# Performance work log

Hardware: AMD Instinct MI355X
Metric: run time of the kernel (lower is better)

Reference implementation:

```python
import jax, jax.numpy as jnp
import numpy as np

N = 50000      # nodes
E = 400000     # edges (before self loops)
IN = 128       # in_channels
H = 4          # num_heads (layers 1-2)
C = 32         # hidden_dim per head
HID = H * C    # 128 total hidden
CLS = 40       # num_classes (out_heads = 1)
EPS = 1e-5     # BatchNorm eps
SLOPE = 0.2    # LeakyReLU negative slope (PyG GATConv default)


def setup_inputs() -> dict:
    key = jax.random.key(0)
    ks = jax.random.split(key, 24)
    rn = lambda k, shp, s: jax.random.normal(k, shp, jnp.float32) * s
    x = jax.random.normal(ks[0], (N, IN), jnp.float32)
    src = jax.random.randint(ks[1], (E,), 0, N)
    dst = jax.random.randint(ks[2], (E,), 0, N)
    src = jnp.where(src == dst, (src + 1) % N, src)  # no pre-existing self loops
    edge_index = jnp.stack([src, dst]).astype(jnp.int32)
    inp = dict(x=x, edge_index=edge_index)
    # conv1: in IN -> H heads x C
    inp['W1'] = rn(ks[3], (IN, H * C), 1.0 / np.sqrt(IN))
    inp['as1'] = rn(ks[4], (H, C), 0.1)
    inp['ad1'] = rn(ks[5], (H, C), 0.1)
    inp['b1'] = rn(ks[6], (H * C,), 0.02)
    # conv2: HID -> H x C
    inp['W2'] = rn(ks[7], (HID, H * C), 1.0 / np.sqrt(HID))
    inp['as2'] = rn(ks[8], (H, C), 0.1)
    inp['ad2'] = rn(ks[9], (H, C), 0.1)
    inp['b2'] = rn(ks[10], (H * C,), 0.02)
    # conv3: HID -> 1 head x CLS, concat=False
    inp['W3'] = rn(ks[11], (HID, CLS), 1.0 / np.sqrt(HID))
    inp['as3'] = rn(ks[12], (1, CLS), 0.1)
    inp['ad3'] = rn(ks[13], (1, CLS), 0.1)
    inp['b3'] = rn(ks[14], (CLS,), 0.02)
    # residual projection
    inp['Wres'] = rn(ks[15], (IN, HID), 1.0 / np.sqrt(IN))
    # BatchNorm (eval mode: running stats)
    inp['g1'] = 1.0 + rn(ks[16], (HID,), 0.1)
    inp['be1'] = rn(ks[17], (HID,), 0.1)
    inp['m1'] = rn(ks[18], (HID,), 0.1)
    inp['v1'] = 1.0 + jax.random.uniform(ks[19], (HID,), jnp.float32) * 0.5
    inp['g2'] = 1.0 + rn(ks[20], (HID,), 0.1)
    inp['be2'] = rn(ks[21], (HID,), 0.1)
    inp['m2'] = rn(ks[22], (HID,), 0.1)
    inp['v2'] = 1.0 + jax.random.uniform(ks[23], (HID,), jnp.float32) * 0.5
    return inp


def _gat_conv(h, src, dst, W, a_src, a_dst, bias, heads, out_ch, concat):
    """PyG-style GATConv (eval: attention dropout off), self loops already in src/dst."""
    n = h.shape[0]
    xw = (h @ W).reshape(n, heads, out_ch)                    # [N,H,C]
    e_src = jnp.sum(xw * a_src, axis=-1)                      # [N,H]
    e_dst = jnp.sum(xw * a_dst, axis=-1)                      # [N,H]
    e = jax.nn.leaky_relu(e_src[src] + e_dst[dst], SLOPE)     # [E',H]
    # segment softmax over incoming edges of each dst node
    mseg = jax.ops.segment_max(e, dst, num_segments=n)        # [N,H]
    ex = jnp.exp(e - mseg[dst])
    den = jax.ops.segment_sum(ex, dst, num_segments=n)
    alpha = ex / den[dst]                                     # [E',H]
    out = jax.ops.segment_sum(alpha[:, :, None] * xw[src], dst, num_segments=n)  # [N,H,C]
    out = out.reshape(n, heads * out_ch) if concat else out.mean(axis=1)
    return out + bias


def _bn(h, g, b, m, v):
    return (h - m) * jax.lax.rsqrt(v + EPS) * g + b


def reference(x, edge_index, W1, as1, ad1, b1, W2, as2, ad2, b2,
              W3, as3, ad3, b3, Wres, g1, be1, m1, v1, g2, be2, m2, v2):
    n = x.shape[0]
    loop = jnp.arange(n, dtype=edge_index.dtype)
    src = jnp.concatenate([edge_index[0], loop])  # add self loops (PyG default)
    dst = jnp.concatenate([edge_index[1], loop])
    x0 = x
    h = _gat_conv(x0, src, dst, W1, as1, ad1, b1, H, C, True)
    h = jax.nn.elu(_bn(h, g1, be1, m1, v1) + x0 @ Wres)
    h_res = h
    h = _gat_conv(h, src, dst, W2, as2, ad2, b2, H, C, True)
    h = jax.nn.elu(_bn(h, g2, be2, m2, v2) + h_res)
    logits = _gat_conv(h, src, dst, W3, as3, ad3, b3, 1, CLS, False)
    return logits
```

## Files before the change

### kernel.cpp

```cpp
#include <hip/hip_runtime.h>
#include <hip/hip_bf16.h>

#define THREADS 256

typedef __attribute__((ext_vector_type(8))) short bfrag;
typedef __attribute__((ext_vector_type(4))) float f32x4;

__device__ inline unsigned short f2b(float v) {
    __hip_bfloat16 b = __float2bfloat16(v);
    return *reinterpret_cast<unsigned short*>(&b);
}
__device__ inline float b2f(unsigned short u) {
    return __uint_as_float(((unsigned)u) << 16);
}
__device__ inline float rdv(const void* p, int off, bool isbf) {
    return isbf ? b2f(((const unsigned short*)p)[off]) : ((const float*)p)[off];
}

__global__ void detect_kernel(const unsigned short* __restrict__ x, int n, int* flag) {
    __shared__ int cnt;
    if (threadIdx.x == 0) cnt = 0;
    __syncthreads();
    int local = 0;
    for (int i = threadIdx.x; i < n; i += THREADS) {
        unsigned ex = (x[i] >> 7) & 0xFF;
        if (ex == 0xFF || ex >= 134 || (ex > 0 && ex <= 100)) local++;
    }
    atomicAdd(&cnt, local);
    __syncthreads();
    if (threadIdx.x == 0) *flag = (cnt * 8 > n) ? 0 : 1;
}

struct InPtrs { const void* p[23]; };

__global__ void prep_kernel(InPtrs in, const int* __restrict__ flag,
                            unsigned short* __restrict__ Wl1, unsigned short* __restrict__ Wl2,
                            unsigned short* __restrict__ WlR, unsigned short* __restrict__ Wl3,
                            float* __restrict__ bnsc1, float* __restrict__ bnsh1,
                            float* __restrict__ bnsc2, float* __restrict__ bnsh2,
                            float* __restrict__ AS1f, float* __restrict__ AD1f,
                            float* __restrict__ AS2f, float* __restrict__ AD2f,
                            float* __restrict__ AS3f, float* __restrict__ AD3f,
                            float* __restrict__ B3f, unsigned short* __restrict__ xb,
                            int N, const int* __restrict__ ei, int* __restrict__ deg,
                            int E, int CB) {
    bool isbf = (*flag != 0);
    int b = blockIdx.x;
    if (b < 27) {
        const void* Wv; unsigned short* o; int cols, tt;
        if (b < 8)       { Wv = in.p[2];  o = Wl1; cols = 128; tt = b; }
        else if (b < 16) { Wv = in.p[6];  o = Wl2; cols = 128; tt = b - 8; }
        else if (b < 24) { Wv = in.p[14]; o = WlR; cols = 128; tt = b - 16; }
        else             { Wv = in.p[10]; o = Wl3; cols = 40;  tt = b - 24; }
        int id = tt * 256 + threadIdx.x;
        int t = id >> 8, ks = (id >> 6) & 3, l = id & 63;
        int q = l >> 4, n = l & 15;
        int c = t * 16 + n;
#pragma unroll
        for (int j = 0; j < 8; ++j) {
            int k = ks * 32 + q * 8 + j;
            float v = (c < cols) ? rdv(Wv, k * cols + c, isbf) : 0.f;
            o[id * 8 + j] = f2b(v);
        }
    } else if (b == 27) {
        int c = threadIdx.x;
        if (c < 128) {
            float s = rdv(in.p[15], c, isbf) * rsqrtf(rdv(in.p[18], c, isbf) + 1e-5f);
            bnsc1[c] = s;
            bnsh1[c] = rdv(in.p[16], c, isbf) - rdv(in.p[17], c, isbf) * s +
                       rdv(in.p[5], c, isbf) * s;
            AS1f[c] = rdv(in.p[3], c, isbf);
            AD1f[c] = rdv(in.p[4], c, isbf);
            AS2f[c] = rdv(in.p[7], c, isbf);
            AD2f[c] = rdv(in.p[8], c, isbf);
        } else {
            int d = c - 128;
            float s = rdv(in.p[19], d, isbf) * rsqrtf(rdv(in.p[22], d, isbf) + 1e-5f);
            bnsc2[d] = s;
            bnsh2[d] = rdv(in.p[20], d, isbf) - rdv(in.p[21], d, isbf) * s +
                       rdv(in.p[9], d, isbf) * s;
            if (d < 40) {
                AS3f[d] = rdv(in.p[11], d, isbf);
                AD3f[d] = rdv(in.p[12], d, isbf);
                B3f[d] = rdv(in.p[13], d, isbf);
            }
        }
    } else if (b < 28 + CB) {
        int i = (b - 28) * 256 + threadIdx.x;
        if (i < E + N) {
            int d = (i < E) ? ei[E + i] : (i - E);
            atomicAdd(&deg[d], 1);
        }
    } else {
        if (isbf) return;
        const float* xf = (const float*)in.p[0];
        int total = N * 128;
        int stride = (gridDim.x - 28 - CB) * 256;
        for (int i = (b - 28 - CB) * 256 + threadIdx.x; i < total; i += stride)
            xb[i] = f2b(xf[i]);
    }
}

__global__ void bsum_kernel(const int* __restrict__ deg, int* __restrict__ bsum, int N) {
    int idx = blockIdx.x * 256 + threadIdx.x;
    int lane = threadIdx.x & 63, wv = threadIdx.x >> 6;
    int v = (idx < N) ? deg[idx] : 0;
#pragma unroll
    for (int o = 1; o < 64; o <<= 1) v += __shfl_xor(v, o, 64);
    __shared__ int ws[4];
    if (lane == 0) ws[wv] = v;
    __syncthreads();
    if (threadIdx.x == 0) bsum[blockIdx.x] = ws[0] + ws[1] + ws[2] + ws[3];
}

__global__ __launch_bounds__(1024) void bscan_kernel(const int* __restrict__ bsum,
                                                     int* __restrict__ boff, int nb) {
    __shared__ int ws[16];
    int tid = threadIdx.x, lane = tid & 63, wv = tid >> 6;
    int v = (tid < nb) ? bsum[tid] : 0;
    int sc = v;
#pragma unroll
    for (int o = 1; o < 64; o <<= 1) {
        int t = __shfl_up(sc, o, 64);
        if (lane >= o) sc += t;
    }
    if (lane == 63) ws[wv] = sc;
    __syncthreads();
    int add = 0;
#pragma unroll
    for (int k = 0; k < 16; ++k) add += (k < wv) ? ws[k] : 0;
    if (tid < nb) boff[tid] = add + sc - v;
}

__global__ void scanw_kernel(const int* __restrict__ deg, const int* __restrict__ boff,
                             int* __restrict__ row_ptr, int* __restrict__ pos, int N) {
    int idx = blockIdx.x * 256 + threadIdx.x;
    int lane = threadIdx.x & 63, wv = threadIdx.x >> 6;
    int v = (idx < N) ? deg[idx] : 0;
    int sc = v;
#pragma unroll
    for (int o = 1; o < 64; o <<= 1) {
        int t = __shfl_up(sc, o, 64);
        if (lane >= o) sc += t;
    }
    __shared__ int ws[4];
    if (lane == 63) ws[wv] = sc;
    __syncthreads();
    int add = boff[blockIdx.x];
#pragma unroll
    for (int k = 0; k < 4; ++k) add += (k < wv) ? ws[k] : 0;
    int excl = add + sc - v;
    if (idx < N) {
        pos[idx] = excl;
        row_ptr[idx + 1] = excl + v;
    }
    if (idx == 0) row_ptr[0] = 0;
}

__global__ void scatter_kernel(const int* __restrict__ ei, int* __restrict__ pos,
                               int* __restrict__ csr, int E, int N) {
    int e = blockIdx.x * THREADS + threadIdx.x;
    if (e >= E + N) return;
    int s, d;
    if (e < E) { s = ei[e]; d = ei[E + e]; }
    else { s = e - E; d = s; }
    int p = atomicAdd(&pos[d], 1);
    csr[p] = s;
}

template <int COLT, int HEADS, bool ES>
__global__ __launch_bounds__(256) void gemm_mfma(
    const unsigned short* __restrict__ A, const unsigned short* __restrict__ Wg,
    const float* __restrict__ as_f, const float* __restrict__ ad_f,
    unsigned short* __restrict__ out, int ldc, int cols,
    float* __restrict__ es, float* __restrict__ ed, int N) {
    __shared__ __align__(16) unsigned short Wls[COLT * 2048];
    int tid = threadIdx.x;
    {
        const float4* src = (const float4*)Wg;
        float4* dst = (float4*)Wls;
#pragma unroll
        for (int i = 0; i < COLT; ++i) dst[tid + i * 256] = src[tid + i * 256];
    }
    __syncthreads();
    int w = tid >> 6, lane = tid & 63;
    int n = lane & 15, q = lane >> 4;
    int row0 = blockIdx.x * 64 + w * 16;
    int ar = row0 + n; ar = ar < N ? ar : N - 1;
    f32x4 acc[COLT];
#pragma unroll
    for (int t = 0; t < COLT; ++t) acc[t] = (f32x4){0.f, 0.f, 0.f, 0.f};
    const unsigned short* arow = A + (size_t)ar * 128;
#pragma unroll
    for (int ks = 0; ks < 4; ++ks) {
        bfrag a = *reinterpret_cast<const bfrag*>(arow + ks * 32 + q * 8);
#pragma unroll
        for (int t = 0; t < COLT; ++t) {
            bfrag b = *reinterpret_cast<const bfrag*>(&Wls[((t * 4 + ks) * 64 + lane) * 8]);
            acc[t] = __builtin_amdgcn_mfma_f32_16x16x32_bf16(a, b, acc[t], 0, 0, 0);
        }
    }
    if (ES) {
        float asv[COLT], adv[COLT];
#pragma unroll
        for (int t = 0; t < COLT; ++t) {
            int c = t * 16 + n;
            asv[t] = (c < cols) ? as_f[c] : 0.f;
            adv[t] = (c < cols) ? ad_f[c] : 0.f;
        }
#pragma unroll
        for (int r = 0; r < 4; ++r) {
            float pe[HEADS], pd[HEADS];
#pragma unroll
            for (int h = 0; h < HEADS; ++h) { pe[h] = 0.f; pd[h] = 0.f; }
#pragma unroll
            for (int t = 0; t < COLT; ++t) {
                int h = (HEADS == 4) ? (t >> 1) : 0;
                pe[h] = fmaf(acc[t][r], asv[t], pe[h]);
                pd[h] = fmaf(acc[t][r], adv[t], pd[h]);
            }
#pragma unroll
            for (int h = 0; h < HEADS; ++h) {
#pragma unroll
                for (int o = 1; o < 16; o <<= 1) {
                    pe[h] += __shfl_xor(pe[h], o, 64);
                    pd[h] += __shfl_xor(pd[h], o, 64);
                }
            }
            int row = row0 + q * 4 + r;
            if (n == 0 && row < N) {
#pragma unroll
                for (int h = 0; h < HEADS; ++h) {
                    es[(size_t)row * HEADS + h] = pe[h];
                    ed[(size_t)row * HEADS + h] = pd[h];
                }
            }
        }
    }
#pragma unroll
    for (int t = 0; t < COLT; ++t) {
        int col = t * 16 + n;
        if (col < cols) {
#pragma unroll
            for (int r = 0; r < 4; ++r) {
                int row = row0 + q * 4 + r;
                if (row < N) out[(size_t)row * ldc + col] = f2b(acc[t][r]);
            }
        }
    }
}

__global__ __launch_bounds__(256) void gemm_dual(
    const unsigned short* __restrict__ Araw, const unsigned short* __restrict__ Acvt,
    const int* __restrict__ flag,
    const unsigned short* __restrict__ Wg1, const unsigned short* __restrict__ WgR,
    const float* __restrict__ as_f, const float* __restrict__ ad_f,
    unsigned short* __restrict__ xwb, unsigned short* __restrict__ resb,
    float* __restrict__ es, float* __restrict__ ed, int N) {
    __shared__ __align__(16) unsigned short Wls[16 * 2048];
    int tid = threadIdx.x;
    {
        const float4* s1 = (const float4*)Wg1;
        const float4* s2 = (const float4*)WgR;
        float4* dst = (float4*)Wls;
#pragma unroll
        for (int i = 0; i < 8; ++i) dst[tid + i * 256] = s1[tid + i * 256];
#pragma unroll
        for (int i = 0; i < 8; ++i) dst[2048 + tid + i * 256] = s2[tid + i * 256];
    }
    const unsigned short* A = (*flag) ? Araw : Acvt;
    __syncthreads();
    int w = tid >> 6, lane = tid & 63;
    int n = lane & 15, q = lane >> 4;
    int row0 = blockIdx.x * 64 + w * 16;
    int ar = row0 + n; ar = ar < N ? ar : N - 1;
    f32x4 acc[16];
#pragma unroll
    for (int t = 0; t < 16; ++t) acc[t] = (f32x4){0.f, 0.f, 0.f, 0.f};
    const unsigned short* arow = A + (size_t)ar * 128;
#pragma unroll
    for (int ks = 0; ks < 4; ++ks) {
        bfrag a = *reinterpret_cast<const bfrag*>(arow + ks * 32 + q * 8);
#pragma unroll
        for (int t = 0; t < 8; ++t) {
            bfrag b = *reinterpret_cast<const bfrag*>(&Wls[((t * 4 + ks) * 64 + lane) * 8]);
            acc[t] = __builtin_amdgcn_mfma_f32_16x16x32_bf16(a, b, acc[t], 0, 0, 0);
        }
#pragma unroll
        for (int t = 0; t < 8; ++t) {
            bfrag b = *reinterpret_cast<const bfrag*>(&Wls[16384 + ((t * 4 + ks) * 64 + lane) * 8]);
            acc[8 + t] = __builtin_amdgcn_mfma_f32_16x16x32_bf16(a, b, acc[8 + t], 0, 0, 0);
        }
    }
    float asv[8], adv[8];
#pragma unroll
    for (int t = 0; t < 8; ++t) {
        int c = t * 16 + n;
        asv[t] = as_f[c];
        adv[t] = ad_f[c];
    }
#pragma unroll
    for (int r = 0; r < 4; ++r) {
        float pe[4] = {0.f, 0.f, 0.f, 0.f}, pd[4] = {0.f, 0.f, 0.f, 0.f};
#pragma unroll
        for (int t = 0; t < 8; ++t) {
            int h = t >> 1;
            pe[h] = fmaf(acc[t][r], asv[t], pe[h]);
            pd[h] = fmaf(acc[t][r], adv[t], pd[h]);
        }
#pragma unroll
        for (int h = 0; h < 4; ++h) {
#pragma unroll
            for (int o = 1; o < 16; o <<= 1) {
                pe[h] += __shfl_xor(pe[h], o, 64);
                pd[h] += __shfl_xor(pd[h], o, 64);
            }
        }
        int row = row0 + q * 4 + r;
        if (n == 0 && row < N) {
#pragma unroll
            for (int h = 0; h < 4; ++h) {
                es[(size_t)row * 4 + h] = pe[h];
                ed[(size_t)row * 4 + h] = pd[h];
            }
        }
    }
#pragma unroll
    for (int t = 0; t < 8; ++t) {
        int col = t * 16 + n;
#pragma unroll
        for (int r = 0; r < 4; ++r) {
            int row = row0 + q * 4 + r;
            if (row < N) {
                xwb[(size_t)row * 128 + col] = f2b(acc[t][r]);
                resb[(size_t)row * 128 + col] = f2b(acc[8 + t][r]);
            }
        }
    }
}

__global__ __launch_bounds__(256) void agg128_fused(
    const unsigned short* __restrict__ xwb, const float* __restrict__ es,
    const float* __restrict__ ed, const int* __restrict__ row_ptr,
    const int* __restrict__ csr, const float* __restrict__ bnsc,
    const float* __restrict__ bnsh, const unsigned short* __restrict__ resb,
    unsigned short* __restrict__ outb, int N) {
    int w = threadIdx.x >> 6, lane = threadIdx.x & 63;
    int node = blockIdx.x * 4 + w;
    if (node >= N) return;
    int h = lane >> 4;
    int c0 = lane * 2;
    float edl = ed[node * 4 + h];
    int start = __builtin_amdgcn_readfirstlane(row_ptr[node]);
    int end = __builtin_amdgcn_readfirstlane(row_ptr[node + 1]);
    float den = 0.f, a0 = 0.f, a1 = 0.f;
    for (int jb = start; jb < end; jb += 16) {
        int su[16];
#pragma unroll
        for (int u = 0; u < 16; ++u) {
            int idx = jb + u;
            idx = idx < end - 1 ? idx : end - 1;
            su[u] = csr[idx];
        }
        unsigned uu[16];
        float ev[16];
#pragma unroll
        for (int u = 0; u < 16; ++u) {
            uu[u] = *(const unsigned*)(xwb + (size_t)su[u] * 128 + c0);
            ev[u] = es[su[u] * 4 + h];
        }
#pragma unroll
        for (int u = 0; u < 16; ++u) {
            float e = ev[u] + edl;
            e = e > 0.f ? e : 0.2f * e;
            float wg = __expf(e);
            wg = (jb + u < end) ? wg : 0.f;
            den += wg;
            a0 = fmaf(wg, __uint_as_float(uu[u] << 16), a0);
            a1 = fmaf(wg, __uint_as_float(uu[u] & 0xffff0000u), a1);
        }
    }
    float inv = 1.f / den;
    float2 sc = *(const float2*)(bnsc + c0);
    float2 sh = *(const float2*)(bnsh + c0);
    unsigned ur = *(const unsigned*)(resb + (size_t)node * 128 + c0);
    float v0 = fmaf(a0 * inv, sc.x, sh.x) + __uint_as_float(ur << 16);
    float v1 = fmaf(a1 * inv, sc.y, sh.y) + __uint_as_float(ur & 0xffff0000u);
    v0 = v0 > 0.f ? v0 : expm1f(v0);
    v1 = v1 > 0.f ? v1 : expm1f(v1);
    unsigned pk = (unsigned)f2b(v0) | ((unsigned)f2b(v1) << 16);
    *(unsigned*)(outb + (size_t)node * 128 + c0) = pk;
}

__global__ __launch_bounds__(256) void agg40_kernel(
    const unsigned short* __restrict__ xw3b, const float* __restrict__ es3,
    const float* __restrict__ ed3, const int* __restrict__ row_ptr,
    const int* __restrict__ csr, const float* __restrict__ b3,
    void* __restrict__ out, const int* __restrict__ flag, int N) {
    int w = threadIdx.x >> 6, lane = threadIdx.x & 63;
    int node = blockIdx.x * 4 + w;
    if (node >= N) return;
    int i16 = lane & 15;
    int g = lane >= 40 ? 2 : (lane >= 20 ? 1 : 0);
    int cp = lane - g * 20;
    int c0 = cp * 2; c0 = c0 > 38 ? 38 : c0;
    float edl = ed3[node];
    int start = row_ptr[node], end = row_ptr[node + 1];
    float den = 0.f, a0 = 0.f, a1 = 0.f;
    for (int jb = start; jb < end; jb += 16) {
        int cnt = end - jb; cnt = cnt < 16 ? cnt : 16;
        int sv = csr[jb + (i16 < cnt ? i16 : 0)];
        unsigned uu[6];
#pragma unroll
        for (int t = 0; t < 6; ++t) {
            int slot = 3 * t + g; slot = slot < 15 ? slot : 15;
            int s = __shfl(sv, slot, 64);
            uu[t] = *(const unsigned*)(xw3b + (size_t)s * 40 + c0);
        }
        float wgl = 0.f;
        if (i16 < cnt) {
            float e = es3[sv] + edl;
            e = e > 0.f ? e : 0.2f * e;
            wgl = __expf(e);
        }
        float d = wgl;
        d += __shfl_xor(d, 1, 64);
        d += __shfl_xor(d, 2, 64);
        d += __shfl_xor(d, 4, 64);
        d += __shfl_xor(d, 8, 64);
        den += d;
#pragma unroll
        for (int t = 0; t < 6; ++t) {
            int slot = 3 * t + g;
            int sl = slot < 15 ? slot : 15;
            float wg = __shfl(wgl, sl, 64);
            if (slot >= cnt) wg = 0.f;
            a0 = fmaf(wg, __uint_as_float(uu[t] << 16), a0);
            a1 = fmaf(wg, __uint_as_float(uu[t] & 0xffff0000u), a1);
        }
    }
    float t0 = __shfl(a0, (lane + 20) & 63, 64);
    float t1 = __shfl(a0, (lane + 40) & 63, 64);
    float u0 = __shfl(a1, (lane + 20) & 63, 64);
    float u1 = __shfl(a1, (lane + 40) & 63, 64);
    a0 += t0 + t1;
    a1 += u0 + u1;
    if (lane < 20) {
        float inv = 1.f / den;
        float v0 = a0 * inv + b3[c0];
        float v1 = a1 * inv + b3[c0 + 1];
        size_t eoff = (size_t)node * 40 + c0;
        if (*flag) {
            unsigned pk = (unsigned)f2b(v0) | ((unsigned)f2b(v1) << 16);
            *(unsigned*)((unsigned short*)out + eoff) = pk;
        } else {
            *(float2*)((float*)out + eoff) = make_float2(v0, v1);
        }
    }
}

extern "C" void kernel_launch(void* const* d_in, const int* in_sizes, int n_in,
                              void* d_out, int out_size, void* d_ws, size_t ws_size,
                              hipStream_t stream) {
    (void)n_in; (void)out_size; (void)ws_size;
    const int N = in_sizes[0] / 128;
    const int E = in_sizes[1] / 2;
    const int EPN = E + N;
    const int NB = (N + 255) / 256;
    const int CB = (EPN + 255) / 256;
    char* base = (char*)d_ws;
    size_t off = 0;
    auto alloc = [&](size_t bytes) -> char* {
        char* p = base + off;
        off = (off + bytes + 255) & ~(size_t)255;
        return p;
    };
    int* flag = (int*)alloc(4);
    int* deg = (int*)alloc((size_t)N * 4);
    int* row_ptr = (int*)alloc((size_t)(N + 1) * 4);
    int* pos = (int*)alloc((size_t)N * 4);
    int* bsum = (int*)alloc((size_t)NB * 4);
    int* boff = (int*)alloc((size_t)NB * 4);
    int* csr = (int*)alloc((size_t)EPN * 4);
    float* bnsc1 = (float*)alloc(512); float* bnsh1 = (float*)alloc(512);
    float* bnsc2 = (float*)alloc(512); float* bnsh2 = (float*)alloc(512);
    float* AS1f = (float*)alloc(512); float* AD1f = (float*)alloc(512);
    float* AS2f = (float*)alloc(512); float* AD2f = (float*)alloc(512);
    float* AS3f = (float*)alloc(256); float* AD3f = (float*)alloc(256);
    float* B3f = (float*)alloc(256);
    unsigned short* Wl1 = (unsigned short*)alloc(32768);
    unsigned short* Wl2 = (unsigned short*)alloc(32768);
    unsigned short* WlR = (unsigned short*)alloc(32768);
    unsigned short* Wl3 = (unsigned short*)alloc(12288);
    unsigned short* xb = (unsigned short*)alloc((size_t)N * 128 * 2);
    unsigned short* xwb = (unsigned short*)alloc((size_t)N * 128 * 2);
    unsigned short* h1b = (unsigned short*)alloc((size_t)N * 128 * 2);
    unsigned short* resb = (unsigned short*)alloc((size_t)N * 128 * 2);
    float* es = (float*)alloc((size_t)N * 4 * 4);
    float* ed = (float*)alloc((size_t)N * 4 * 4);

    const int* ei = (const int*)d_in[1];

    hipMemsetAsync(deg, 0, (size_t)N * 4, stream);
    detect_kernel<<<1, THREADS, 0, stream>>>((const unsigned short*)d_in[0], 4096, flag);

    InPtrs ip;
    for (int t = 0; t < 23; t++) ip.p[t] = d_in[t];
    prep_kernel<<<28 + CB + 1024, THREADS, 0, stream>>>(ip, flag, Wl1, Wl2, WlR, Wl3,
                                                        bnsc1, bnsh1, bnsc2, bnsh2,
                                                        AS1f, AD1f, AS2f, AD2f,
                                                        AS3f, AD3f, B3f, xb, N, ei, deg, E, CB);

    bsum_kernel<<<NB, 256, 0, stream>>>(deg, bsum, N);
    bscan_kernel<<<1, 1024, 0, stream>>>(bsum, boff, NB);
    scanw_kernel<<<NB, 256, 0, stream>>>(deg, boff, row_ptr, pos, N);
    scatter_kernel<<<(EPN + THREADS - 1) / THREADS, THREADS, 0, stream>>>(ei, pos, csr, E, N);

    int gemmGrid = (N + 63) / 64;
    int aggGrid = (N + 3) / 4;

    gemm_dual<<<gemmGrid, 256, 0, stream>>>((const unsigned short*)d_in[0], xb, flag,
                                            Wl1, WlR, AS1f, AD1f, xwb, resb, es, ed, N);
    agg128_fused<<<aggGrid, 256, 0, stream>>>(xwb, es, ed, row_ptr, csr,
                                              bnsc1, bnsh1, resb, h1b, N);
    gemm_mfma<8, 4, true><<<gemmGrid, 256, 0, stream>>>(
        h1b, Wl2, AS2f, AD2f, xwb, 128, 128, es, ed, N);
    unsigned short* h2b = resb;
    agg128_fused<<<aggGrid, 256, 0, stream>>>(xwb, es, ed, row_ptr, csr,
                                              bnsc2, bnsh2, h1b, h2b, N);
    gemm_mfma<3, 1, true><<<gemmGrid, 256, 0, stream>>>(
        h2b, Wl3, AS3f, AD3f, xwb, 40, 40, es, ed, N);
    agg40_kernel<<<aggGrid, 256, 0, stream>>>(xwb, es, ed, row_ptr, csr, B3f,
                                              d_out, flag, N);
}
```

Measured before the change: 288.5 us.

## Fuse CSR build into one cooperative kernel and convert fp32 input inside GEMM

Replaces the memset, detect, prep, block-sum, block-scan, scan-write and scatter launches with a single cooperative kernel of 512 blocks that uses grid-wide syncs between phases. Each block computes its own offset by summing the block sums before it, instead of running a separate scan. The first GEMM now reads the fp32 input directly and converts it to bf16 in registers, which removes the separate conversion pass and its intermediate buffer. The aim is to cut launch overhead and memory traffic, at the cost of grid.sync latency and a redundant prefix sum in each block.

```diff
diff --git a/kernel.cpp b/kernel.cpp
--- a/kernel.cpp
+++ b/kernel.cpp
@@ -1,5 +1,8 @@
 #include <hip/hip_runtime.h>
 #include <hip/hip_bf16.h>
+#include <hip/hip_cooperative_groups.h>
+
+namespace cg = cooperative_groups;
 
 #define THREADS 256
 
@@ -17,42 +20,49 @@
     return isbf ? b2f(((const unsigned short*)p)[off]) : ((const float*)p)[off];
 }
 
-__global__ void detect_kernel(const unsigned short* __restrict__ x, int n, int* flag) {
-    __shared__ int cnt;
-    if (threadIdx.x == 0) cnt = 0;
-    __syncthreads();
-    int local = 0;
-    for (int i = threadIdx.x; i < n; i += THREADS) {
-        unsigned ex = (x[i] >> 7) & 0xFF;
-        if (ex == 0xFF || ex >= 134 || (ex > 0 && ex <= 100)) local++;
-    }
-    atomicAdd(&cnt, local);
-    __syncthreads();
-    if (threadIdx.x == 0) *flag = (cnt * 8 > n) ? 0 : 1;
-}
-
 struct InPtrs { const void* p[23]; };
 
-__global__ void prep_kernel(InPtrs in, const int* __restrict__ flag,
-                            unsigned short* __restrict__ Wl1, unsigned short* __restrict__ Wl2,
-                            unsigned short* __restrict__ WlR, unsigned short* __restrict__ Wl3,
-                            float* __restrict__ bnsc1, float* __restrict__ bnsh1,
-                            float* __restrict__ bnsc2, float* __restrict__ bnsh2,
-                            float* __restrict__ AS1f, float* __restrict__ AD1f,
-                            float* __restrict__ AS2f, float* __restrict__ AD2f,
-                            float* __restrict__ AS3f, float* __restrict__ AD3f,
-                            float* __restrict__ B3f, unsigned short* __restrict__ xb,
-                            int N, const int* __restrict__ ei, int* __restrict__ deg,
-                            int E, int CB) {
-    bool isbf = (*flag != 0);
-    int b = blockIdx.x;
+__global__ __launch_bounds__(256, 2) void coop_prep(
+    InPtrs in, int* __restrict__ flag,
+    unsigned short* __restrict__ Wl1, unsigned short* __restrict__ Wl2,
+    unsigned short* __restrict__ WlR, unsigned short* __restrict__ Wl3,
+    float* __restrict__ bnsc1, float* __restrict__ bnsh1,
+    float* __restrict__ bnsc2, float* __restrict__ bnsh2,
+    float* __restrict__ AS1f, float* __restrict__ AD1f,
+    float* __restrict__ AS2f, float* __restrict__ AD2f,
+    float* __restrict__ AS3f, float* __restrict__ AD3f, float* __restrict__ B3f,
+    int* __restrict__ deg, int* __restrict__ bsum,
+    int* __restrict__ row_ptr, int* __restrict__ pos, int* __restrict__ csr,
+    const int* __restrict__ ei, int N, int E, int NB) {
+    cg::grid_group grid = cg::this_grid();
+    int b = blockIdx.x, tid = threadIdx.x, G = gridDim.x;
+    __shared__ int sred[8];
+
+    for (int i = b * 256 + tid; i < N; i += G * 256) deg[i] = 0;
+    if (b == 0) {
+        const unsigned short* x = (const unsigned short*)in.p[0];
+        int local = 0;
+        for (int i = tid; i < 4096; i += 256) {
+            unsigned ex = (x[i] >> 7) & 0xFF;
+            if (ex == 0xFF || ex >= 134 || (ex > 0 && ex <= 100)) local++;
+        }
+#pragma unroll
+        for (int o = 1; o < 64; o <<= 1) local += __shfl_xor(local, o, 64);
+        if ((tid & 63) == 0) sred[tid >> 6] = local;
+        __syncthreads();
+        if (tid == 0)
+            *flag = ((sred[0] + sred[1] + sred[2] + sred[3]) * 8 > 4096) ? 0 : 1;
+    }
+    grid.sync();
+
     if (b < 27) {
+        bool isbf = (*flag != 0);
         const void* Wv; unsigned short* o; int cols, tt;
         if (b < 8)       { Wv = in.p[2];  o = Wl1; cols = 128; tt = b; }
         else if (b < 16) { Wv = in.p[6];  o = Wl2; cols = 128; tt = b - 8; }
         else if (b < 24) { Wv = in.p[14]; o = WlR; cols = 128; tt = b - 16; }
         else             { Wv = in.p[10]; o = Wl3; cols = 40;  tt = b - 24; }
-        int id = tt * 256 + threadIdx.x;
+        int id = tt * 256 + tid;
         int t = id >> 8, ks = (id >> 6) & 3, l = id & 63;
         int q = l >> 4, n = l & 15;
         int c = t * 16 + n;
@@ -63,7 +73,8 @@
             o[id * 8 + j] = f2b(v);
         }
     } else if (b == 27) {
-        int c = threadIdx.x;
+        bool isbf = (*flag != 0);
+        int c = tid;
         if (c < 128) {
             float s = rdv(in.p[15], c, isbf) * rsqrtf(rdv(in.p[18], c, isbf) + 1e-5f);
             bnsc1[c] = s;
@@ -85,87 +96,67 @@
                 B3f[d] = rdv(in.p[13], d, isbf);
             }
         }
-    } else if (b < 28 + CB) {
-        int i = (b - 28) * 256 + threadIdx.x;
-        if (i < E + N) {
+    } else {
+        int stride = (G - 28) * 256;
+        for (int i = (b - 28) * 256 + tid; i < E + N; i += stride) {
             int d = (i < E) ? ei[E + i] : (i - E);
             atomicAdd(&deg[d], 1);
         }
-    } else {
-        if (isbf) return;
-        const float* xf = (const float*)in.p[0];
-        int total = N * 128;
-        int stride = (gridDim.x - 28 - CB) * 256;
-        for (int i = (b - 28 - CB) * 256 + threadIdx.x; i < total; i += stride)
-            xb[i] = f2b(xf[i]);
-    }
-}
-
-__global__ void bsum_kernel(const int* __restrict__ deg, int* __restrict__ bsum, int N) {
-    int idx = blockIdx.x * 256 + threadIdx.x;
-    int lane = threadIdx.x & 63, wv = threadIdx.x >> 6;
-    int v = (idx < N) ? deg[idx] : 0;
-#pragma unroll
-    for (int o = 1; o < 64; o <<= 1) v += __shfl_xor(v, o, 64);
-    __shared__ int ws[4];
-    if (lane == 0) ws[wv] = v;
-    __syncthreads();
-    if (threadIdx.x == 0) bsum[blockIdx.x] = ws[0] + ws[1] + ws[2] + ws[3];
-}
-
-__global__ __launch_bounds__(1024) void bscan_kernel(const int* __restrict__ bsum,
-                                                     int* __restrict__ boff, int nb) {
-    __shared__ int ws[16];
-    int tid = threadIdx.x, lane = tid & 63, wv = tid >> 6;
-    int v = (tid < nb) ? bsum[tid] : 0;
-    int sc = v;
-#pragma unroll
-    for (int o = 1; o < 64; o <<= 1) {
-        int t = __shfl_up(sc, o, 64);
-        if (lane >= o) sc += t;
-    }
-    if (lane == 63) ws[wv] = sc;
-    __syncthreads();
-    int add = 0;
-#pragma unroll
-    for (int k = 0; k < 16; ++k) add += (k < wv) ? ws[k] : 0;
-    if (tid < nb) boff[tid] = add + sc - v;
-}
-
-__global__ void scanw_kernel(const int* __restrict__ deg, const int* __restrict__ boff,
-                             int* __restrict__ row_ptr, int* __restrict__ pos, int N) {
-    int idx = blockIdx.x * 256 + threadIdx.x;
-    int lane = threadIdx.x & 63, wv = threadIdx.x >> 6;
-    int v = (idx < N) ? deg[idx] : 0;
-    int sc = v;
-#pragma unroll
-    for (int o = 1; o < 64; o <<= 1) {
-        int t = __shfl_up(sc, o, 64);
-        if (lane >= o) sc += t;
-    }
-    __shared__ int ws[4];
-    if (lane == 63) ws[wv] = sc;
-    __syncthreads();
-    int add = boff[blockIdx.x];
-#pragma unroll
-    for (int k = 0; k < 4; ++k) add += (k < wv) ? ws[k] : 0;
-    int excl = add + sc - v;
-    if (idx < N) {
-        pos[idx] = excl;
-        row_ptr[idx + 1] = excl + v;
-    }
-    if (idx == 0) row_ptr[0] = 0;
-}
-
-__global__ void scatter_kernel(const int* __restrict__ ei, int* __restrict__ pos,
-                               int* __restrict__ csr, int E, int N) {
-    int e = blockIdx.x * THREADS + threadIdx.x;
-    if (e >= E + N) return;
-    int s, d;
-    if (e < E) { s = ei[e]; d = ei[E + e]; }
-    else { s = e - E; d = s; }
-    int p = atomicAdd(&pos[d], 1);
-    csr[p] = s;
+    }
+    grid.sync();
+
+    for (int cb = b; cb < NB; cb += G) {
+        int idx = cb * 256 + tid;
+        int v = (idx < N) ? deg[idx] : 0;
+        int s = v;
+#pragma unroll
+        for (int o = 1; o < 64; o <<= 1) s += __shfl_xor(s, o, 64);
+        if ((tid & 63) == 0) sred[tid >> 6] = s;
+        __syncthreads();
+        if (tid == 0) bsum[cb] = sred[0] + sred[1] + sred[2] + sred[3];
+        __syncthreads();
+    }
+    grid.sync();
+
+    for (int cb = b; cb < NB; cb += G) {
+        int acc = 0;
+        for (int t = tid; t < cb; t += 256) acc += bsum[t];
+#pragma unroll
+        for (int o = 1; o < 64; o <<= 1) acc += __shfl_xor(acc, o, 64);
+        if ((tid & 63) == 0) sred[tid >> 6] = acc;
+        __syncthreads();
+        int boff = sred[0] + sred[1] + sred[2] + sred[3];
+        int idx = cb * 256 + tid;
+        int v = (idx < N) ? deg[idx] : 0;
+        int lane = tid & 63, wv = tid >> 6;
+        int sc = v;
+#pragma unroll
+        for (int o = 1; o < 64; o <<= 1) {
+            int t2 = __shfl_up(sc, o, 64);
+            if (lane >= o) sc += t2;
+        }
+        if (lane == 63) sred[4 + wv] = sc;
+        __syncthreads();
+        int add = boff;
+#pragma unroll
+        for (int k = 0; k < 4; ++k) add += (k < wv) ? sred[4 + k] : 0;
+        int excl = add + sc - v;
+        if (idx < N) {
+            pos[idx] = excl;
+            row_ptr[idx + 1] = excl + v;
+        }
+        if (idx == 0) row_ptr[0] = 0;
+        __syncthreads();
+    }
+    grid.sync();
+
+    for (int i = b * 256 + tid; i < E + N; i += G * 256) {
+        int s, d;
+        if (i < E) { s = ei[i]; d = ei[E + i]; }
+        else { s = i - E; d = s; }
+        int p = atomicAdd(&pos[d], 1);
+        csr[p] = s;
+    }
 }
 
 template <int COLT, int HEADS, bool ES>
@@ -251,8 +242,7 @@
 }
 
 __global__ __launch_bounds__(256) void gemm_dual(
-    const unsigned short* __restrict__ Araw, const unsigned short* __restrict__ Acvt,
-    const int* __restrict__ flag,
+    const void* __restrict__ Ain, const int* __restrict__ flag,
     const unsigned short* __restrict__ Wg1, const unsigned short* __restrict__ WgR,
     const float* __restrict__ as_f, const float* __restrict__ ad_f,
     unsigned short* __restrict__ xwb, unsigned short* __restrict__ resb,
@@ -268,28 +258,46 @@
 #pragma unroll
         for (int i = 0; i < 8; ++i) dst[2048 + tid + i * 256] = s2[tid + i * 256];
     }
-    const unsigned short* A = (*flag) ? Araw : Acvt;
+    bool isbf = (*flag != 0);
     __syncthreads();
     int w = tid >> 6, lane = tid & 63;
     int n = lane & 15, q = lane >> 4;
     int row0 = blockIdx.x * 64 + w * 16;
     int ar = row0 + n; ar = ar < N ? ar : N - 1;
+    bfrag a[4];
+    if (isbf) {
+        const unsigned short* arow = (const unsigned short*)Ain + (size_t)ar * 128;
+#pragma unroll
+        for (int ks = 0; ks < 4; ++ks)
+            a[ks] = *reinterpret_cast<const bfrag*>(arow + ks * 32 + q * 8);
+    } else {
+        const float* arow = (const float*)Ain + (size_t)ar * 128;
+#pragma unroll
+        for (int ks = 0; ks < 4; ++ks) {
+            float4 f0 = *reinterpret_cast<const float4*>(arow + ks * 32 + q * 8);
+            float4 f1 = *reinterpret_cast<const float4*>(arow + ks * 32 + q * 8 + 4);
+            bfrag t;
+            t[0] = (short)f2b(f0.x); t[1] = (short)f2b(f0.y);
+            t[2] = (short)f2b(f0.z); t[3] = (short)f2b(f0.w);
+            t[4] = (short)f2b(f1.x); t[5] = (short)f2b(f1.y);
+            t[6] = (short)f2b(f1.z); t[7] = (short)f2b(f1.w);
+            a[ks] = t;
+        }
+    }
     f32x4 acc[16];
 #pragma unroll
     for (int t = 0; t < 16; ++t) acc[t] = (f32x4){0.f, 0.f, 0.f, 0.f};
-    const unsigned short* arow = A + (size_t)ar * 128;
 #pragma unroll
     for (int ks = 0; ks < 4; ++ks) {
-        bfrag a = *reinterpret_cast<const bfrag*>(arow + ks * 32 + q * 8);
 #pragma unroll
         for (int t = 0; t < 8; ++t) {
             bfrag b = *reinterpret_cast<const bfrag*>(&Wls[((t * 4 + ks) * 64 + lane) * 8]);
-            acc[t] = __builtin_amdgcn_mfma_f32_16x16x32_bf16(a, b, acc[t], 0, 0, 0);
+            acc[t] = __builtin_amdgcn_mfma_f32_16x16x32_bf16(a[ks], b, acc[t], 0, 0, 0);
         }
 #pragma unroll
         for (int t = 0; t < 8; ++t) {
             bfrag b = *reinterpret_cast<const bfrag*>(&Wls[16384 + ((t * 4 + ks) * 64 + lane) * 8]);
-            acc[8 + t] = __builtin_amdgcn_mfma_f32_16x16x32_bf16(a, b, acc[8 + t], 0, 0, 0);
+            acc[8 + t] = __builtin_amdgcn_mfma_f32_16x16x32_bf16(a[ks], b, acc[8 + t], 0, 0, 0);
         }
     }
     float asv[8], adv[8];
@@ -467,7 +475,6 @@
     const int E = in_sizes[1] / 2;
     const int EPN = E + N;
     const int NB = (N + 255) / 256;
-    const int CB = (EPN + 255) / 256;
     char* base = (char*)d_ws;
     size_t off = 0;
     auto alloc = [&](size_t bytes) -> char* {
@@ -480,7 +487,6 @@
     int* row_ptr = (int*)alloc((size_t)(N + 1) * 4);
     int* pos = (int*)alloc((size_t)N * 4);
     int* bsum = (int*)alloc((size_t)NB * 4);
-    int* boff = (int*)alloc((size_t)NB * 4);
     int* csr = (int*)alloc((size_t)EPN * 4);
     float* bnsc1 = (float*)alloc(512); float* bnsh1 = (float*)alloc(512);
     float* bnsc2 = (float*)alloc(512); float* bnsh2 = (float*)alloc(512);
@@ -492,7 +498,6 @@
     unsigned short* Wl2 = (unsigned short*)alloc(32768);
     unsigned short* WlR = (unsigned short*)alloc(32768);
     unsigned short* Wl3 = (unsigned short*)alloc(12288);
-    unsigned short* xb = (unsigned short*)alloc((size_t)N * 128 * 2);
     unsigned short* xwb = (unsigned short*)alloc((size_t)N * 128 * 2);
     unsigned short* h1b = (unsigned short*)alloc((size_t)N * 128 * 2);
     unsigned short* resb = (unsigned short*)alloc((size_t)N * 128 * 2);
@@ -501,26 +506,23 @@
 
     const int* ei = (const int*)d_in[1];
 
-    hipMemsetAsync(deg, 0, (size_t)N * 4, stream);
-    detect_kernel<<<1, THREADS, 0, stream>>>((const unsigned short*)d_in[0], 4096, flag);
-
     InPtrs ip;
     for (int t = 0; t < 23; t++) ip.p[t] = d_in[t];
-    prep_kernel<<<28 + CB + 1024, THREADS, 0, stream>>>(ip, flag, Wl1, Wl2, WlR, Wl3,
-                                                        bnsc1, bnsh1, bnsc2, bnsh2,
-                                                        AS1f, AD1f, AS2f, AD2f,
-                                                        AS3f, AD3f, B3f, xb, N, ei, deg, E, CB);
-
-    bsum_kernel<<<NB, 256, 0, stream>>>(deg, bsum, N);
-    bscan_kernel<<<1, 1024, 0, stream>>>(bsum, boff, NB);
-    scanw_kernel<<<NB, 256, 0, stream>>>(deg, boff, row_ptr, pos, N);
-    scatter_kernel<<<(EPN + THREADS - 1) / THREADS, THREADS, 0, stream>>>(ei, pos, csr, E, N);
+
+    int Nv = N, Ev = E, NBv = NB;
+    const int* eip = ei;
+    void* cargs[] = {&ip, &flag, &Wl1, &Wl2, &WlR, &Wl3,
+                     &bnsc1, &bnsh1, &bnsc2, &bnsh2,
+                     &AS1f, &AD1f, &AS2f, &AD2f, &AS3f, &AD3f, &B3f,
+                     &deg, &bsum, &row_ptr, &pos, &csr, &eip, &Nv, &Ev, &NBv};
+    hipLaunchCooperativeKernel((const void*)coop_prep, dim3(512), dim3(256),
+                               cargs, 0, stream);
 
     int gemmGrid = (N + 63) / 64;
     int aggGrid = (N + 3) / 4;
 
-    gemm_dual<<<gemmGrid, 256, 0, stream>>>((const unsigned short*)d_in[0], xb, flag,
-                                            Wl1, WlR, AS1f, AD1f, xwb, resb, es, ed, N);
+    gemm_dual<<<gemmGrid, 256, 0, stream>>>(d_in[0], flag, Wl1, WlR, AS1f, AD1f,
+                                            xwb, resb, es, ed, N);
     agg128_fused<<<aggGrid, 256, 0, stream>>>(xwb, es, ed, row_ptr, csr,
                                               bnsc1, bnsh1, resb, h1b, N);
     gemm_mfma<8, 4, true><<<gemmGrid, 256, 0, stream>>>(
```

New measurement: 520.5 us. 1.8x slower.

## Fold attention vectors into weights and use decoupled-lookback single-pass scan

Applied to the files above, without the earlier changes.

Precomputes W·a_src and W·a_dst as extra weight columns, so the attention logits come straight out of the MFMA accumulators instead of per-row FMA and shuffle reductions in the GEMM epilogue. It also merges the three-kernel degree scan into one decoupled-lookback scan kernel and folds the dtype-detection kernel into prep_kernel, with every block that needs the flag recomputing it redundantly. This removes several kernel launches and epilogue work, at the cost of redundant detection reads, spin-waiting in the scan, and bf16 rounding of the folded attention weights.

```diff
diff --git a/kernel.cpp b/kernel.cpp
--- a/kernel.cpp
+++ b/kernel.cpp
@@ -17,76 +17,79 @@
     return isbf ? b2f(((const unsigned short*)p)[off]) : ((const float*)p)[off];
 }
 
-__global__ void detect_kernel(const unsigned short* __restrict__ x, int n, int* flag) {
-    __shared__ int cnt;
-    if (threadIdx.x == 0) cnt = 0;
-    __syncthreads();
-    int local = 0;
-    for (int i = threadIdx.x; i < n; i += THREADS) {
-        unsigned ex = (x[i] >> 7) & 0xFF;
-        if (ex == 0xFF || ex >= 134 || (ex > 0 && ex <= 100)) local++;
-    }
-    atomicAdd(&cnt, local);
-    __syncthreads();
-    if (threadIdx.x == 0) *flag = (cnt * 8 > n) ? 0 : 1;
-}
-
 struct InPtrs { const void* p[23]; };
 
-__global__ void prep_kernel(InPtrs in, const int* __restrict__ flag,
+__global__ void prep_kernel(InPtrs in, int* __restrict__ flag,
                             unsigned short* __restrict__ Wl1, unsigned short* __restrict__ Wl2,
                             unsigned short* __restrict__ WlR, unsigned short* __restrict__ Wl3,
                             float* __restrict__ bnsc1, float* __restrict__ bnsh1,
                             float* __restrict__ bnsc2, float* __restrict__ bnsh2,
-                            float* __restrict__ AS1f, float* __restrict__ AD1f,
-                            float* __restrict__ AS2f, float* __restrict__ AD2f,
-                            float* __restrict__ AS3f, float* __restrict__ AD3f,
                             float* __restrict__ B3f, unsigned short* __restrict__ xb,
                             int N, const int* __restrict__ ei, int* __restrict__ deg,
                             int E, int CB) {
-    bool isbf = (*flag != 0);
-    int b = blockIdx.x;
-    if (b < 27) {
-        const void* Wv; unsigned short* o; int cols, tt;
-        if (b < 8)       { Wv = in.p[2];  o = Wl1; cols = 128; tt = b; }
-        else if (b < 16) { Wv = in.p[6];  o = Wl2; cols = 128; tt = b - 8; }
-        else if (b < 24) { Wv = in.p[14]; o = WlR; cols = 128; tt = b - 16; }
-        else             { Wv = in.p[10]; o = Wl3; cols = 40;  tt = b - 24; }
-        int id = tt * 256 + threadIdx.x;
-        int t = id >> 8, ks = (id >> 6) & 3, l = id & 63;
+    int b = blockIdx.x, tid = threadIdx.x;
+    __shared__ int sred[4];
+    bool isbf = false;
+    bool needf = (b < 30) || (b >= 30 + CB);
+    if (needf) {
+        const unsigned short* x = (const unsigned short*)in.p[0];
+        int local = 0;
+        for (int i = tid; i < 4096; i += 256) {
+            unsigned ex = (x[i] >> 7) & 0xFF;
+            if (ex == 0xFF || ex >= 134 || (ex > 0 && ex <= 100)) local++;
+        }
+#pragma unroll
+        for (int o = 1; o < 64; o <<= 1) local += __shfl_xor(local, o, 64);
+        if ((tid & 63) == 0) sred[tid >> 6] = local;
+        __syncthreads();
+        int cnt = sred[0] + sred[1] + sred[2] + sred[3];
+        isbf = !(cnt * 8 > 4096);
+    }
+    if (b < 29) {
+        const void *Wv, *asp = 0, *adp = 0; unsigned short* o; int cols, C = 0, FH = 0, tt;
+        if (b < 9)       { Wv = in.p[2];  asp = in.p[3];  adp = in.p[4];  o = Wl1; cols = 128; C = 32; FH = 4; tt = b; }
+        else if (b < 18) { Wv = in.p[6];  asp = in.p[7];  adp = in.p[8];  o = Wl2; cols = 128; C = 32; FH = 4; tt = b - 9; }
+        else if (b < 26) { Wv = in.p[14];                                 o = WlR; cols = 128;                 tt = b - 18; }
+        else             { Wv = in.p[10]; asp = in.p[11]; adp = in.p[12]; o = Wl3; cols = 40;  C = 40; FH = 1; tt = b - 26; }
+        int id = tt * 256 + tid;
+        int ks = (id >> 6) & 3, l = id & 63;
         int q = l >> 4, n = l & 15;
-        int c = t * 16 + n;
+        int c = tt * 16 + n;
 #pragma unroll
         for (int j = 0; j < 8; ++j) {
             int k = ks * 32 + q * 8 + j;
-            float v = (c < cols) ? rdv(Wv, k * cols + c, isbf) : 0.f;
+            float v = 0.f;
+            if (c < cols) {
+                v = rdv(Wv, k * cols + c, isbf);
+            } else if (FH && c < cols + 2 * FH) {
+                int dn = c - cols;
+                int h = dn < FH ? dn : dn - FH;
+                const void* av = dn < FH ? asp : adp;
+                float s = 0.f;
+                for (int cc = 0; cc < C; ++cc)
+                    s += rdv(Wv, k * cols + h * C + cc, isbf) * rdv(av, h * C + cc, isbf);
+                v = s;
+            }
             o[id * 8 + j] = f2b(v);
         }
-    } else if (b == 27) {
-        int c = threadIdx.x;
+    } else if (b == 29) {
+        int c = tid;
         if (c < 128) {
             float s = rdv(in.p[15], c, isbf) * rsqrtf(rdv(in.p[18], c, isbf) + 1e-5f);
             bnsc1[c] = s;
             bnsh1[c] = rdv(in.p[16], c, isbf) - rdv(in.p[17], c, isbf) * s +
                        rdv(in.p[5], c, isbf) * s;
-            AS1f[c] = rdv(in.p[3], c, isbf);
-            AD1f[c] = rdv(in.p[4], c, isbf);
-            AS2f[c] = rdv(in.p[7], c, isbf);
-            AD2f[c] = rdv(in.p[8], c, isbf);
         } else {
             int d = c - 128;
             float s = rdv(in.p[19], d, isbf) * rsqrtf(rdv(in.p[22], d, isbf) + 1e-5f);
             bnsc2[d] = s;
             bnsh2[d] = rdv(in.p[20], d, isbf) - rdv(in.p[21], d, isbf) * s +
                        rdv(in.p[9], d, isbf) * s;
-            if (d < 40) {
-                AS3f[d] = rdv(in.p[11], d, isbf);
-                AD3f[d] = rdv(in.p[12], d, isbf);
-                B3f[d] = rdv(in.p[13], d, isbf);
-            }
-        }
-    } else if (b < 28 + CB) {
-        int i = (b - 28) * 256 + threadIdx.x;
+            if (d < 40) B3f[d] = rdv(in.p[13], d, isbf);
+        }
+        if (tid == 0) *flag = isbf ? 1 : 0;
+    } else if (b < 30 + CB) {
+        int i = (b - 30) * 256 + tid;
         if (i < E + N) {
             int d = (i < E) ? ei[E + i] : (i - E);
             atomicAdd(&deg[d], 1);
@@ -95,29 +98,21 @@
         if (isbf) return;
         const float* xf = (const float*)in.p[0];
         int total = N * 128;
-        int stride = (gridDim.x - 28 - CB) * 256;
-        for (int i = (b - 28 - CB) * 256 + threadIdx.x; i < total; i += stride)
+        int stride = (gridDim.x - 30 - CB) * 256;
+        for (int i = (b - 30 - CB) * 256 + tid; i < total; i += stride)
             xb[i] = f2b(xf[i]);
     }
 }
 
-__global__ void bsum_kernel(const int* __restrict__ deg, int* __restrict__ bsum, int N) {
-    int idx = blockIdx.x * 256 + threadIdx.x;
-    int lane = threadIdx.x & 63, wv = threadIdx.x >> 6;
+__global__ __launch_bounds__(256) void scan_kernel(
+    const int* __restrict__ deg, unsigned long long* __restrict__ look,
+    int* __restrict__ row_ptr, int* __restrict__ pos, int N) {
+    int b = blockIdx.x, tid = threadIdx.x;
+    int lane = tid & 63, wv = tid >> 6;
+    __shared__ int ws[4];
+    __shared__ int s_off;
+    int idx = b * 256 + tid;
     int v = (idx < N) ? deg[idx] : 0;
-#pragma unroll
-    for (int o = 1; o < 64; o <<= 1) v += __shfl_xor(v, o, 64);
-    __shared__ int ws[4];
-    if (lane == 0) ws[wv] = v;
-    __syncthreads();
-    if (threadIdx.x == 0) bsum[blockIdx.x] = ws[0] + ws[1] + ws[2] + ws[3];
-}
-
-__global__ __launch_bounds__(1024) void bscan_kernel(const int* __restrict__ bsum,
-                                                     int* __restrict__ boff, int nb) {
-    __shared__ int ws[16];
-    int tid = threadIdx.x, lane = tid & 63, wv = tid >> 6;
-    int v = (tid < nb) ? bsum[tid] : 0;
     int sc = v;
 #pragma unroll
     for (int o = 1; o < 64; o <<= 1) {
@@ -126,27 +121,39 @@
     }
     if (lane == 63) ws[wv] = sc;
     __syncthreads();
-    int add = 0;
-#pragma unroll
-    for (int k = 0; k < 16; ++k) add += (k < wv) ? ws[k] : 0;
-    if (tid < nb) boff[tid] = add + sc - v;
-}
-
-__global__ void scanw_kernel(const int* __restrict__ deg, const int* __restrict__ boff,
-                             int* __restrict__ row_ptr, int* __restrict__ pos, int N) {
-    int idx = blockIdx.x * 256 + threadIdx.x;
-    int lane = threadIdx.x & 63, wv = threadIdx.x >> 6;
-    int v = (idx < N) ? deg[idx] : 0;
-    int sc = v;
-#pragma unroll
-    for (int o = 1; o < 64; o <<= 1) {
-        int t = __shfl_up(sc, o, 64);
-        if (lane >= o) sc += t;
-    }
-    __shared__ int ws[4];
-    if (lane == 63) ws[wv] = sc;
+    int tot = ws[0] + ws[1] + ws[2] + ws[3];
+    if (tid == 0)
+        atomicExch(&look[b], (1ULL << 32) | (unsigned)tot);
+    if (wv == 0) {
+        int run = 0;
+        if (b > 0) {
+            int base = b - 1;
+            for (;;) {
+                int i = base - lane;
+                unsigned long long st = (i >= 0) ? atomicAdd(&look[i], 0ULL)
+                                                 : (2ULL << 32);
+                int status = (int)(st >> 32);
+                int val = (int)(st & 0xffffffffULL);
+                unsigned long long bp = __ballot(status == 2);
+                unsigned long long bz = __ballot(status == 0);
+                int fp = bp ? (__ffsll(bp) - 1) : 64;
+                int fz = bz ? (__ffsll(bz) - 1) : 64;
+                if (fz < fp) continue;
+                int contrib = (lane <= fp) ? val : 0;
+#pragma unroll
+                for (int o = 1; o < 64; o <<= 1) contrib += __shfl_xor(contrib, o, 64);
+                run += contrib;
+                if (fp < 64) break;
+                base -= 64;
+            }
+        }
+        if (lane == 0) {
+            s_off = run;
+            atomicExch(&look[b], (2ULL << 32) | (unsigned)(run + tot));
+        }
+    }
     __syncthreads();
-    int add = boff[blockIdx.x];
+    int add = s_off;
 #pragma unroll
     for (int k = 0; k < 4; ++k) add += (k < wv) ? ws[k] : 0;
     int excl = add + sc - v;
@@ -168,10 +175,9 @@
     csr[p] = s;
 }
 
-template <int COLT, int HEADS, bool ES>
+template <int COLT, int HEADS, int ESCOL>
 __global__ __launch_bounds__(256) void gemm_mfma(
     const unsigned short* __restrict__ A, const unsigned short* __restrict__ Wg,
-    const float* __restrict__ as_f, const float* __restrict__ ad_f,
     unsigned short* __restrict__ out, int ldc, int cols,
     float* __restrict__ es, float* __restrict__ ed, int N) {
     __shared__ __align__(16) unsigned short Wls[COLT * 2048];
@@ -200,41 +206,15 @@
             acc[t] = __builtin_amdgcn_mfma_f32_16x16x32_bf16(a, b, acc[t], 0, 0, 0);
         }
     }
-    if (ES) {
-        float asv[COLT], adv[COLT];
-#pragma unroll
-        for (int t = 0; t < COLT; ++t) {
-            int c = t * 16 + n;
-            asv[t] = (c < cols) ? as_f[c] : 0.f;
-            adv[t] = (c < cols) ? ad_f[c] : 0.f;
-        }
-#pragma unroll
-        for (int r = 0; r < 4; ++r) {
-            float pe[HEADS], pd[HEADS];
-#pragma unroll
-            for (int h = 0; h < HEADS; ++h) { pe[h] = 0.f; pd[h] = 0.f; }
-#pragma unroll
-            for (int t = 0; t < COLT; ++t) {
-                int h = (HEADS == 4) ? (t >> 1) : 0;
-                pe[h] = fmaf(acc[t][r], asv[t], pe[h]);
-                pd[h] = fmaf(acc[t][r], adv[t], pd[h]);
-            }
-#pragma unroll
-            for (int h = 0; h < HEADS; ++h) {
-#pragma unroll
-                for (int o = 1; o < 16; o <<= 1) {
-                    pe[h] += __shfl_xor(pe[h], o, 64);
-                    pd[h] += __shfl_xor(pd[h], o, 64);
-                }
-            }
-            int row = row0 + q * 4 + r;
-            if (n == 0 && row < N) {
-#pragma unroll
-                for (int h = 0; h < HEADS; ++h) {
-                    es[(size_t)row * HEADS + h] = pe[h];
-                    ed[(size_t)row * HEADS + h] = pd[h];
-                }
-            }
+    constexpr int TE = ESCOL >> 4, NE = ESCOL & 15;
+    int dn = n - NE;
+#pragma unroll
+    for (int r = 0; r < 4; ++r) {
+        int row = row0 + q * 4 + r;
+        if (row < N) {
+            if (dn >= 0 && dn < HEADS) es[(size_t)row * HEADS + dn] = acc[TE][r];
+            else if (dn >= HEADS && dn < 2 * HEADS)
+                ed[(size_t)row * HEADS + (dn - HEADS)] = acc[TE][r];
         }
     }
 #pragma unroll
@@ -254,7 +234,6 @@
     const unsigned short* __restrict__ Araw, const unsigned short* __restrict__ Acvt,
     const int* __restrict__ flag,
     const unsigned short* __restrict__ Wg1, const unsigned short* __restrict__ WgR,
-    const float* __restrict__ as_f, const float* __restrict__ ad_f,
     unsigned short* __restrict__ xwb, unsigned short* __restrict__ resb,
     float* __restrict__ es, float* __restrict__ ed, int N) {
     __shared__ __align__(16) unsigned short Wls[16 * 2048];
@@ -274,9 +253,10 @@
     int n = lane & 15, q = lane >> 4;
     int row0 = blockIdx.x * 64 + w * 16;
     int ar = row0 + n; ar = ar < N ? ar : N - 1;
-    f32x4 acc[16];
+    f32x4 acc[16], accE;
 #pragma unroll
     for (int t = 0; t < 16; ++t) acc[t] = (f32x4){0.f, 0.f, 0.f, 0.f};
+    accE = (f32x4){0.f, 0.f, 0.f, 0.f};
     const unsigned short* arow = A + (size_t)ar * 128;
 #pragma unroll
     for (int ks = 0; ks < 4; ++ks) {
@@ -286,43 +266,20 @@
             bfrag b = *reinterpret_cast<const bfrag*>(&Wls[((t * 4 + ks) * 64 + lane) * 8]);
             acc[t] = __builtin_amdgcn_mfma_f32_16x16x32_bf16(a, b, acc[t], 0, 0, 0);
         }
+        bfrag be = *reinterpret_cast<const bfrag*>(Wg1 + ((size_t)(32 + ks) * 64 + lane) * 8);
+        accE = __builtin_amdgcn_mfma_f32_16x16x32_bf16(a, be, accE, 0, 0, 0);
 #pragma unroll
         for (int t = 0; t < 8; ++t) {
             bfrag b = *reinterpret_cast<const bfrag*>(&Wls[16384 + ((t * 4 + ks) * 64 + lane) * 8]);
             acc[8 + t] = __builtin_amdgcn_mfma_f32_16x16x32_bf16(a, b, acc[8 + t], 0, 0, 0);
         }
     }
-    float asv[8], adv[8];
-#pragma unroll
-    for (int t = 0; t < 8; ++t) {
-        int c = t * 16 + n;
-        asv[t] = as_f[c];
-        adv[t] = ad_f[c];
-    }
 #pragma unroll
     for (int r = 0; r < 4; ++r) {
-        float pe[4] = {0.f, 0.f, 0.f, 0.f}, pd[4] = {0.f, 0.f, 0.f, 0.f};
-#pragma unroll
-        for (int t = 0; t < 8; ++t) {
-            int h = t >> 1;
-            pe[h] = fmaf(acc[t][r], asv[t], pe[h]);
-            pd[h] = fmaf(acc[t][r], adv[t], pd[h]);
-        }
-#pragma unroll
-        for (int h = 0; h < 4; ++h) {
-#pragma unroll
-            for (int o = 1; o < 16; o <<= 1) {
-                pe[h] += __shfl_xor(pe[h], o, 64);
-                pd[h] += __shfl_xor(pd[h], o, 64);
-            }
-        }
         int row = row0 + q * 4 + r;
-        if (n == 0 && row < N) {
-#pragma unroll
-            for (int h = 0; h < 4; ++h) {
-                es[(size_t)row * 4 + h] = pe[h];
-                ed[(size_t)row * 4 + h] = pd[h];
-            }
+        if (row < N) {
+            if (n < 4) es[(size_t)row * 4 + n] = accE[r];
+            else if (n < 8) ed[(size_t)row * 4 + (n - 4)] = accE[r];
         }
     }
 #pragma unroll
@@ -476,20 +433,19 @@
         return p;
     };
     int* flag = (int*)alloc(4);
-    int* deg = (int*)alloc((size_t)N * 4);
+    size_t degB = (size_t)N * 4;
+    degB = (degB + 7) & ~(size_t)7;
+    char* zreg = alloc(degB + (size_t)NB * 8);
+    int* deg = (int*)zreg;
+    unsigned long long* look = (unsigned long long*)(zreg + degB);
     int* row_ptr = (int*)alloc((size_t)(N + 1) * 4);
     int* pos = (int*)alloc((size_t)N * 4);
-    int* bsum = (int*)alloc((size_t)NB * 4);
-    int* boff = (int*)alloc((size_t)NB * 4);
     int* csr = (int*)alloc((size_t)EPN * 4);
     float* bnsc1 = (float*)alloc(512); float* bnsh1 = (float*)alloc(512);
     float* bnsc2 = (float*)alloc(512); float* bnsh2 = (float*)alloc(512);
-    float* AS1f = (float*)alloc(512); float* AD1f = (float*)alloc(512);
-    float* AS2f = (float*)alloc(512); float* AD2f = (float*)alloc(512);
-    float* AS3f = (float*)alloc(256); float* AD3f = (float*)alloc(256);
     float* B3f = (float*)alloc(256);
-    unsigned short* Wl1 = (unsigned short*)alloc(32768);
-    unsigned short* Wl2 = (unsigned short*)alloc(32768);
+    unsigned short* Wl1 = (unsigned short*)alloc(36864);
+    unsigned short* Wl2 = (unsigned short*)alloc(36864);
     unsigned short* WlR = (unsigned short*)alloc(32768);
     unsigned short* Wl3 = (unsigned short*)alloc(12288);
     unsigned short* xb = (unsigned short*)alloc((size_t)N * 128 * 2);
@@ -501,35 +457,31 @@
 
     const int* ei = (const int*)d_in[1];
 
-    hipMemsetAsync(deg, 0, (size_t)N * 4, stream);
-    detect_kernel<<<1, THREADS, 0, stream>>>((const unsigned short*)d_in[0], 4096, flag);
+    hipMemsetAsync(zreg, 0, degB + (size_t)NB * 8, stream);
 
     InPtrs ip;
     for (int t = 0; t < 23; t++) ip.p[t] = d_in[t];
-    prep_kernel<<<28 + CB + 1024, THREADS, 0, stream>>>(ip, flag, Wl1, Wl2, WlR, Wl3,
+    prep_kernel<<<30 + CB + 1024, THREADS, 0, stream>>>(ip, flag, Wl1, Wl2, WlR, Wl3,
                                                         bnsc1, bnsh1, bnsc2, bnsh2,
-                                                        AS1f, AD1f, AS2f, AD2f,
-                                                        AS3f, AD3f, B3f, xb, N, ei, deg, E, CB);
-
-    bsum_kernel<<<NB, 256, 0, stream>>>(deg, bsum, N);
-    bscan_kernel<<<1, 1024, 0, stream>>>(bsum, boff, NB);
-    scanw_kernel<<<NB, 256, 0, stream>>>(deg, boff, row_ptr, pos, N);
+                                                        B3f, xb, N, ei, deg, E, CB);
+
+    scan_kernel<<<NB, 256, 0, stream>>>(deg, look, row_ptr, pos, N);
     scatter_kernel<<<(EPN + THREADS - 1) / THREADS, THREADS, 0, stream>>>(ei, pos, csr, E, N);
 
     int gemmGrid = (N + 63) / 64;
     int aggGrid = (N + 3) / 4;
 
     gemm_dual<<<gemmGrid, 256, 0, stream>>>((const unsigned short*)d_in[0], xb, flag,
-                                            Wl1, WlR, AS1f, AD1f, xwb, resb, es, ed, N);
+                                            Wl1, WlR, xwb, resb, es, ed, N);
     agg128_fused<<<aggGrid, 256, 0, stream>>>(xwb, es, ed, row_ptr, csr,
                                               bnsc1, bnsh1, resb, h1b, N);
-    gemm_mfma<8, 4, true><<<gemmGrid, 256, 0, stream>>>(
-        h1b, Wl2, AS2f, AD2f, xwb, 128, 128, es, ed, N);
+    gemm_mfma<9, 4, 128><<<gemmGrid, 256, 0, stream>>>(
+        h1b, Wl2, xwb, 128, 128, es, ed, N);
     unsigned short* h2b = resb;
     agg128_fused<<<aggGrid, 256, 0, stream>>>(xwb, es, ed, row_ptr, csr,
                                               bnsc2, bnsh2, h1b, h2b, N);
-    gemm_mfma<3, 1, true><<<gemmGrid, 256, 0, stream>>>(
-        h2b, Wl3, AS3f, AD3f, xwb, 40, 40, es, ed, N);
+    gemm_mfma<3, 1, 40><<<gemmGrid, 256, 0, stream>>>(
+        h2b, Wl3, xwb, 40, 40, es, ed, N);
     agg40_kernel<<<aggGrid, 256, 0, stream>>>(xwb, es, ed, row_ptr, csr, B3f,
                                               d_out, flag, N);
 }
```

New measurement: 308.8 us. 7.0% more time.
